# Kernel tuning notes

Measured on AMD Instinct MI355X. Metric: run time of the kernel, lower is better.

The kernel has to match this reference:

```python
import jax, jax.numpy as jnp
import numpy as np
from jax import lax

N, T, V, E, H, D, B = 16384, 16, 10000, 256, 256, 512, 128


def setup_inputs() -> dict:
    key = jax.random.key(0)
    ks = jax.random.split(key, 12)
    tok = jax.random.randint(ks[0], (N, T), 1, V)
    lens = jax.random.randint(ks[1], (N,), 4, T + 1)
    tok = jnp.where(jnp.arange(T)[None, :] < lens[:, None], tok, 0)  # pad_id = 0
    ast_path_len = jnp.full((B,), N // B, dtype=jnp.int32)  # 128 paths per sample
    u = lambda k, s: jax.random.uniform(k, s, jnp.float32, -0.1, 0.1)
    emb = u(ks[2], (V, E)).at[0].set(0.0)  # padding_idx=0 row zeroed
    return {
        "ast_path": tok,
        "ast_path_len": ast_path_len,
        "emb": emb,
        "W_ih_f": u(ks[3], (4 * H, E)), "W_hh_f": u(ks[4], (4 * H, H)), "b_f": u(ks[5], (4 * H,)),
        "W_ih_b": u(ks[6], (4 * H, E)), "W_hh_b": u(ks[7], (4 * H, H)), "b_b": u(ks[8], (4 * H,)),
        "W_lin": u(ks[9], (D, 2 * H)), "b_lin": jnp.zeros((D,), jnp.float32),
    }


def _lstm_final_h(x_tm, lens, W_ih, W_hh, b, reverse):
    # x_tm: [T, N, E]; returns final hidden state [N, H] honoring per-seq length
    n = x_tm.shape[1]
    h0 = jnp.zeros((n, H), x_tm.dtype)

    def step(carry, xt):
        h, c = carry
        x, t = xt
        gates = x @ W_ih.T + h @ W_hh.T + b  # [N, 4H]
        i, f, g, o = jnp.split(gates, 4, axis=-1)
        c_new = jax.nn.sigmoid(f) * c + jax.nn.sigmoid(i) * jnp.tanh(g)
        h_new = jax.nn.sigmoid(o) * jnp.tanh(c_new)
        m = (t < lens)[:, None]  # packed-sequence semantics: frozen past length
        return (jnp.where(m, h_new, h), jnp.where(m, c_new, c)), None

    (h, _), _ = lax.scan(step, (h0, h0), (x_tm, jnp.arange(x_tm.shape[0])), reverse=reverse)
    return h


def reference(ast_path, ast_path_len, emb, W_ih_f, W_hh_f, b_f, W_ih_b, W_hh_b, b_b, W_lin, b_lin):
    lens = (ast_path != 0).sum(axis=-1)  # pad_id = 0
    x = emb[ast_path]                     # [N, T, E]; dropout is identity at eval
    x_tm = jnp.swapaxes(x, 0, 1)          # [T, N, E]
    h_fwd = _lstm_final_h(x_tm, lens, W_ih_f, W_hh_f, b_f, reverse=False)
    h_bwd = _lstm_final_h(x_tm, lens, W_ih_b, W_hh_b, b_b, reverse=True)
    h_n = jnp.concatenate([h_fwd, h_bwd], axis=1)        # [N, 2H]
    repr_ = h_n @ W_lin.T + b_lin                         # [N, D]
    # segment-mean pooling over path groups (replaces the Python loop)
    n_paths = repr_.shape[0]
    seg_ids = jnp.repeat(jnp.arange(ast_path_len.shape[0]), ast_path_len,
                         total_repeat_length=n_paths)
    sums = jax.ops.segment_sum(repr_, seg_ids, num_segments=ast_path_len.shape[0])
    pooled = sums / ast_path_len[:, None].astype(repr_.dtype)  # [B, D]
    norm = jnp.sqrt(jnp.sum(pooled * pooled, axis=-1, keepdims=True))
    return pooled / jnp.maximum(norm, 1e-5)
```

## Files before the change

kernel.cpp:

```cpp
#include <hip/hip_runtime.h>
#include <stdint.h>

#define N_SEQ 16384
#define T_LEN 16
#define E_DIM 256
#define H_DIM 256
#define K_DIM 512
#define B_SAMP 128
#define V_SIZE 10000

typedef __bf16 bf16x8 __attribute__((ext_vector_type(8)));
typedef float  f32x4  __attribute__((ext_vector_type(4)));

__device__ __forceinline__ unsigned short f2bf(float x) {
  unsigned int u = __float_as_uint(x);
  u = (u + 0x7fffu + ((u >> 16) & 1u)) >> 16;
  return (unsigned short)u;
}
__device__ __forceinline__ float bf2f(unsigned short v) {
  return __uint_as_float(((unsigned int)v) << 16);
}
__device__ __forceinline__ float sigmoidf_(float x) {
  return 1.0f / (1.0f + __expf(-x));
}
__device__ __forceinline__ void glds16(const void* g, const void* l) {
  __builtin_amdgcn_global_load_lds(
      (const __attribute__((address_space(1))) unsigned int*)g,
      (__attribute__((address_space(3))) unsigned int*)l, 16, 0, 0);
}


__global__ __launch_bounds__(256) void k_lens(const int* __restrict__ tok, int* __restrict__ lens) {
  int n = blockIdx.x * 256 + threadIdx.x;
  const int* r = tok + n * T_LEN;
  int c = 0;
#pragma unroll
  for (int t = 0; t < T_LEN; ++t) c += (r[t] != 0);
  lens[n] = c;
}

__global__ __launch_bounds__(256) void k_hist(const int* __restrict__ lens, int* __restrict__ hist) {
  __shared__ int lh[17];
  if (threadIdx.x < 17) lh[threadIdx.x] = 0;
  __syncthreads();
  atomicAdd(&lh[lens[blockIdx.x * 256 + threadIdx.x]], 1);
  __syncthreads();
  if (threadIdx.x < 17) atomicAdd(&hist[threadIdx.x], lh[threadIdx.x]);
}

__global__ void k_offsets(const int* __restrict__ hist, int* __restrict__ cursor, int* __restrict__ cnts) {
  if (threadIdx.x == 0) {
    int off = 0;
    for (int l = 16; l >= 0; --l) { cursor[l] = off; off += hist[l]; }
    for (int t = 0; t < 16; ++t) {
      int c = 0;
      for (int l = t; l <= 16; ++l) c += hist[l];
      cnts[t] = c;
    }
  }
}

__global__ __launch_bounds__(256) void k_scatter(const int* __restrict__ lens, int* __restrict__ cursor,
                                                 int* __restrict__ perm, int* __restrict__ pinv,
                                                 int* __restrict__ plens) {
  int n = blockIdx.x * 256 + threadIdx.x;
  int l = lens[n];
  int pos = atomicAdd(&cursor[l], 1);
  perm[pos] = n;
  pinv[n] = pos;
  plens[pos] = l;
}

__global__ __launch_bounds__(256) void k_embcvt(const float* __restrict__ emb, unsigned short* __restrict__ out) {
  int i = blockIdx.x * 256 + threadIdx.x;
  out[i] = f2bf(emb[i]);
}

__global__ __launch_bounds__(256) void k_wprep(const float* __restrict__ Wih_f, const float* __restrict__ Whh_f,
                                               const float* __restrict__ Wih_b, const float* __restrict__ Whh_b,
                                               unsigned short* __restrict__ wpt_f, unsigned short* __restrict__ wpt_b) {
  int id = blockIdx.x * 256 + threadIdx.x;
  int dir = id >> 19;
  int rem = id & ((1 << 19) - 1);
  int p = rem >> 9;
  int k = rem & 511;
  int nb = p >> 8, wc = (p >> 6) & 3, q = (p >> 4) & 3, jj = p & 15;
  int r = q * 256 + nb * 64 + wc * 16 + jj;
  const float* Wih = dir ? Wih_b : Wih_f;
  const float* Whh = dir ? Whh_b : Whh_f;
  float v = (k < 256) ? Wih[r * 256 + k] : Whh[r * 256 + (k - 256)];
  unsigned short* o = dir ? wpt_b : wpt_f;
  o[p * 512 + k] = f2bf(v);
}


__global__ __launch_bounds__(512, 4)
void k_step(const unsigned short* __restrict__ embbf, const int* __restrict__ tok,
            const int* __restrict__ perm, const int* __restrict__ plens,
            const int* __restrict__ cnts,
            const unsigned short* __restrict__ wpt_f, const unsigned short* __restrict__ wpt_b,
            const float* __restrict__ bias_f, const float* __restrict__ bias_b,
            const unsigned short* __restrict__ hr_f, unsigned short* __restrict__ hw_f,
            const unsigned short* __restrict__ hr_b, unsigned short* __restrict__ hw_b,
            float* __restrict__ c_f, float* __restrict__ c_b,
            int s) {
  const int dir = blockIdx.y;
  const int t = dir ? (T_LEN - 1 - s) : s;
  const int mblk = blockIdx.x >> 2;
  const int m0 = mblk * 128;
  const int cnt = cnts[dir ? (15 - s) : s];
  if (m0 >= cnt) return;

  const int nblk = blockIdx.x & 3;
  const unsigned short* wpt = dir ? wpt_b : wpt_f;
  const float* bias = dir ? bias_b : bias_f;
  const unsigned short* hr = dir ? hr_b : hr_f;
  unsigned short* hw = dir ? hw_b : hw_f;
  float* cc = dir ? c_b : c_f;

  __shared__ __align__(128) unsigned char ldsA[128 * 128];
  __shared__ __align__(128) unsigned char ldsB[256 * 128];

  const int tid = threadIdx.x;
  const int lane = tid & 63;
  const int w = tid >> 6;
  const int wr = w >> 2;
  const int wc = w & 3;

  const int l8 = lane >> 3;
  const int l7 = lane & 7;
  const int arow0 = 16 * w + l8;
  const int arow1 = arow0 + 8;
  const int ach0 = l7 ^ (arow0 & 7);
  const int ach1 = l7 ^ (arow1 & 7);
  const int pn0 = perm[m0 + arow0];
  const int pn1 = perm[m0 + arow1];
  const unsigned aoffE0 = (unsigned)tok[pn0 * T_LEN + t] * E_DIM + ach0 * 8;
  const unsigned aoffE1 = (unsigned)tok[pn1 * T_LEN + t] * E_DIM + ach1 * 8;
  const unsigned aoffH0 = (unsigned)(m0 + arow0) * H_DIM + ach0 * 8;
  const unsigned aoffH1 = (unsigned)(m0 + arow1) * H_DIM + ach1 * 8;
  unsigned boff[4];
#pragma unroll
  for (int j = 0; j < 4; ++j) {
    const int brow = 32 * w + 8 * j + l8;
    const int bch = l7 ^ (brow & 7);
    boff[j] = (unsigned)(nblk * 256 + brow) * K_DIM + bch * 8;
  }

  f32x4 acc[4][4] = {};
  const int frow = lane & 15;
  const int fkq = lane >> 4;

  for (int kt = 0; kt < 8; ++kt) {
    const int k0 = kt * 64;
    if (kt < 4) {
      glds16(embbf + aoffE0 + k0, &ldsA[(16 * w) * 128]);
      glds16(embbf + aoffE1 + k0, &ldsA[(16 * w + 8) * 128]);
    } else {
      glds16(hr + aoffH0 + (k0 - E_DIM), &ldsA[(16 * w) * 128]);
      glds16(hr + aoffH1 + (k0 - E_DIM), &ldsA[(16 * w + 8) * 128]);
    }
#pragma unroll
    for (int j = 0; j < 4; ++j)
      glds16(wpt + boff[j] + k0, &ldsB[(32 * w + 8 * j) * 128]);
    __syncthreads();
#pragma unroll
    for (int ksub = 0; ksub < 2; ++ksub) {
      bf16x8 av[4], bv[4];
#pragma unroll
      for (int fr = 0; fr < 4; ++fr) {
        const int row = wr * 64 + fr * 16 + frow;
        const int ch = (ksub * 4 + fkq) ^ (row & 7);
        av[fr] = *(const bf16x8*)&ldsA[row * 128 + ch * 16];
      }
#pragma unroll
      for (int fc = 0; fc < 4; ++fc) {
        const int row = wc * 64 + fc * 16 + frow;
        const int ch = (ksub * 4 + fkq) ^ (row & 7);
        bv[fc] = *(const bf16x8*)&ldsB[row * 128 + ch * 16];
      }
#pragma unroll
      for (int fr = 0; fr < 4; ++fr)
#pragma unroll
        for (int fc = 0; fc < 4; ++fc)
          acc[fr][fc] = __builtin_amdgcn_mfma_f32_16x16x32_bf16(av[fr], bv[fc], acc[fr][fc], 0, 0, 0);
    }
    __syncthreads();
  }

  const int j = nblk * 64 + wc * 16 + frow;
  const float bi = bias[j], bfv = bias[256 + j], bg = bias[512 + j], bo = bias[768 + j];
#pragma unroll
  for (int fr = 0; fr < 4; ++fr) {
    const int nbase = m0 + wr * 64 + fr * 16 + fkq * 4;
    const int4 ln4 = *(const int4*)&plens[nbase];
    const f32x4 gi = acc[fr][0], gf = acc[fr][1], gg = acc[fr][2], go = acc[fr][3];
#pragma unroll
    for (int r = 0; r < 4; ++r) {
      const int n = nbase + r;
      const int ln = (r == 0) ? ln4.x : (r == 1) ? ln4.y : (r == 2) ? ln4.z : ln4.w;
      const size_t idx = (size_t)n * H_DIM + j;
      if (t < ln) {
        float iv = sigmoidf_(gi[r] + bi);
        float fv = sigmoidf_(gf[r] + bfv);
        float gv = tanhf(gg[r] + bg);
        float ov = sigmoidf_(go[r] + bo);
        float cn = fv * cc[idx] + iv * gv;
        cc[idx] = cn;
        hw[idx] = f2bf(ov * tanhf(cn));
      } else {
        hw[idx] = hr[idx];
      }
    }
  }
}


__global__ __launch_bounds__(256) void k_pool(const unsigned short* __restrict__ hf,
                                              const unsigned short* __restrict__ hb,
                                              const int* __restrict__ pinv,
                                              const int* __restrict__ plen,
                                              float* __restrict__ pooled) {
  const int b = blockIdx.x, tid = threadIdx.x;
  int start = 0;
  for (int i = 0; i < b; ++i) start += plen[i];
  const int cnt = plen[b];
  float s0 = 0.f, s1 = 0.f;
  for (int r = 0; r < cnt; ++r) {
    const size_t pr = (size_t)pinv[start + r];
    s0 += bf2f(hf[pr * H_DIM + tid]);
    s1 += bf2f(hb[pr * H_DIM + tid]);
  }
  float inv = 1.0f / (float)cnt;
  pooled[b * 512 + tid] = s0 * inv;
  pooled[b * 512 + H_DIM + tid] = s1 * inv;
}


__global__ __launch_bounds__(256) void k_final(const float* __restrict__ pooled,
                                               const float* __restrict__ W,
                                               const float* __restrict__ bl,
                                               float* __restrict__ out) {
  const int b = blockIdx.x, tid = threadIdx.x;
  __shared__ float pv[512];
  __shared__ float pre[512];
  __shared__ float red[4];
  pv[tid] = pooled[b * 512 + tid];
  pv[tid + 256] = pooled[b * 512 + 256 + tid];
  __syncthreads();
#pragma unroll
  for (int half = 0; half < 2; ++half) {
    const int dd = tid + half * 256;
    const f32x4* wr = (const f32x4*)(W + (size_t)dd * 512);
    const f32x4* pvv = (const f32x4*)pv;
    float s = bl[dd];
#pragma unroll 4
    for (int k4 = 0; k4 < 128; ++k4) {
      f32x4 wv = wr[k4], xv = pvv[k4];
      s += wv[0] * xv[0] + wv[1] * xv[1] + wv[2] * xv[2] + wv[3] * xv[3];
    }
    pre[dd] = s;
  }
  __syncthreads();
  float ss = pre[tid] * pre[tid] + pre[tid + 256] * pre[tid + 256];
#pragma unroll
  for (int off = 32; off > 0; off >>= 1) ss += __shfl_down(ss, off, 64);
  if ((tid & 63) == 0) red[tid >> 6] = ss;
  __syncthreads();
  float tot = red[0] + red[1] + red[2] + red[3];
  float scale = 1.0f / fmaxf(sqrtf(tot), 1e-5f);
  out[b * 512 + tid] = pre[tid] * scale;
  out[b * 512 + 256 + tid] = pre[tid + 256] * scale;
}


extern "C" void kernel_launch(void* const* d_in, const int* in_sizes, int n_in,
                              void* d_out, int out_size, void* d_ws, size_t ws_size,
                              hipStream_t stream) {
  const int* tok    = (const int*)d_in[0];
  const int* plen   = (const int*)d_in[1];
  const float* emb  = (const float*)d_in[2];
  const float* Wih_f = (const float*)d_in[3];
  const float* Whh_f = (const float*)d_in[4];
  const float* b_f   = (const float*)d_in[5];
  const float* Wih_b = (const float*)d_in[6];
  const float* Whh_b = (const float*)d_in[7];
  const float* b_b   = (const float*)d_in[8];
  const float* Wlin  = (const float*)d_in[9];
  const float* blin  = (const float*)d_in[10];
  float* out = (float*)d_out;

  char* ws = (char*)d_ws;
  size_t off = 0;
  auto alloc = [&](size_t bytes) {
    void* p = ws + off;
    off = (off + bytes + 255) & ~(size_t)255;
    return p;
  };
  unsigned short* embbf = (unsigned short*)alloc((size_t)V_SIZE * E_DIM * 2);
  unsigned short* wptf  = (unsigned short*)alloc((size_t)1024 * K_DIM * 2);
  unsigned short* wptb  = (unsigned short*)alloc((size_t)1024 * K_DIM * 2);
  int* lens             = (int*)alloc((size_t)N_SEQ * 4);
  int* perm             = (int*)alloc((size_t)N_SEQ * 4);
  int* pinv             = (int*)alloc((size_t)N_SEQ * 4);
  int* plens            = (int*)alloc((size_t)N_SEQ * 4);
  int* hist             = (int*)alloc(17 * 4);
  int* cursor           = (int*)alloc(17 * 4);
  int* cnts             = (int*)alloc(16 * 4);
  unsigned short* h0f   = (unsigned short*)alloc((size_t)N_SEQ * H_DIM * 2);
  unsigned short* h1f   = (unsigned short*)alloc((size_t)N_SEQ * H_DIM * 2);
  unsigned short* h0b   = (unsigned short*)alloc((size_t)N_SEQ * H_DIM * 2);
  unsigned short* h1b   = (unsigned short*)alloc((size_t)N_SEQ * H_DIM * 2);
  float* cf             = (float*)alloc((size_t)N_SEQ * H_DIM * 4);
  float* cb             = (float*)alloc((size_t)N_SEQ * H_DIM * 4);
  float* pooled         = (float*)alloc((size_t)B_SAMP * 512 * 4);

  hipMemsetAsync(hist, 0, 17 * 4, stream);
  hipMemsetAsync(h0f, 0, (size_t)N_SEQ * H_DIM * 2, stream);
  hipMemsetAsync(h0b, 0, (size_t)N_SEQ * H_DIM * 2, stream);
  hipMemsetAsync(h1f, 0, (size_t)N_SEQ * H_DIM * 2, stream);
  hipMemsetAsync(h1b, 0, (size_t)N_SEQ * H_DIM * 2, stream);
  hipMemsetAsync(cf, 0, (size_t)N_SEQ * H_DIM * 4, stream);
  hipMemsetAsync(cb, 0, (size_t)N_SEQ * H_DIM * 4, stream);

  k_lens<<<N_SEQ / 256, 256, 0, stream>>>(tok, lens);
  k_hist<<<N_SEQ / 256, 256, 0, stream>>>(lens, hist);
  k_offsets<<<1, 64, 0, stream>>>(hist, cursor, cnts);
  k_scatter<<<N_SEQ / 256, 256, 0, stream>>>(lens, cursor, perm, pinv, plens);
  k_embcvt<<<(V_SIZE * E_DIM) / 256, 256, 0, stream>>>(emb, embbf);
  k_wprep<<<(2 * 1024 * K_DIM) / 256, 256, 0, stream>>>(Wih_f, Whh_f, Wih_b, Whh_b, wptf, wptb);

  dim3 grid(512, 2);
  for (int s = 0; s < T_LEN; ++s) {
    const unsigned short* hrf = (s & 1) ? h1f : h0f;
    unsigned short* hwf       = (s & 1) ? h0f : h1f;
    const unsigned short* hrb = (s & 1) ? h1b : h0b;
    unsigned short* hwb       = (s & 1) ? h0b : h1b;
    k_step<<<grid, 512, 0, stream>>>(embbf, tok, perm, plens, cnts, wptf, wptb, b_f, b_b,
                                     hrf, hwf, hrb, hwb, cf, cb, s);
  }
  k_pool<<<B_SAMP, 256, 0, stream>>>(h0f, h0b, pinv, plen, pooled);
  k_final<<<B_SAMP, 256, 0, stream>>>(pooled, Wlin, blin, out);
}
```

Measured before the change: 943.6 us.

## Fuse per-timestep LSTM launches into one persistent kernel with on-chip state

Replaces the 16 per-timestep k_step launches with a single k_lstm kernel. Each block owns 64 length-sorted rows for one direction and loops over that block's maximum length. The hidden state stays in swizzled LDS and the cell state stays in registers, which removes the global h/c ping-pong buffers, their memsets, and the per-step launch overhead. Weights are now streamed from global/L2 by every block on every step, so cache traffic is higher. Blocks are paired across directions to balance the sorted lengths, and tanh is replaced with an exp-based approximation.

```diff
diff --git a/kernel.cpp b/kernel.cpp
--- a/kernel.cpp
+++ b/kernel.cpp
@@ -11,17 +11,23 @@
 
 typedef __bf16 bf16x8 __attribute__((ext_vector_type(8)));
 typedef float  f32x4  __attribute__((ext_vector_type(4)));
-
-__device__ __forceinline__ unsigned short f2bf(float x) {
+typedef unsigned short u16x8 __attribute__((ext_vector_type(8)));
+typedef unsigned short ush;
+
+__device__ __forceinline__ ush f2bf(float x) {
   unsigned int u = __float_as_uint(x);
   u = (u + 0x7fffu + ((u >> 16) & 1u)) >> 16;
-  return (unsigned short)u;
-}
-__device__ __forceinline__ float bf2f(unsigned short v) {
+  return (ush)u;
+}
+__device__ __forceinline__ float bf2f(ush v) {
   return __uint_as_float(((unsigned int)v) << 16);
 }
 __device__ __forceinline__ float sigmoidf_(float x) {
   return 1.0f / (1.0f + __expf(-x));
+}
+__device__ __forceinline__ float tanhf_(float x) {
+  float e = __expf(2.0f * x);
+  return 1.0f - 2.0f / (e + 1.0f);
 }
 __device__ __forceinline__ void glds16(const void* g, const void* l) {
   __builtin_amdgcn_global_load_lds(
@@ -48,15 +54,10 @@
   if (threadIdx.x < 17) atomicAdd(&hist[threadIdx.x], lh[threadIdx.x]);
 }
 
-__global__ void k_offsets(const int* __restrict__ hist, int* __restrict__ cursor, int* __restrict__ cnts) {
+__global__ void k_offsets(const int* __restrict__ hist, int* __restrict__ cursor) {
   if (threadIdx.x == 0) {
     int off = 0;
     for (int l = 16; l >= 0; --l) { cursor[l] = off; off += hist[l]; }
-    for (int t = 0; t < 16; ++t) {
-      int c = 0;
-      for (int l = t; l <= 16; ++l) c += hist[l];
-      cnts[t] = c;
-    }
   }
 }
 
@@ -71,153 +72,174 @@
   plens[pos] = l;
 }
 
-__global__ __launch_bounds__(256) void k_embcvt(const float* __restrict__ emb, unsigned short* __restrict__ out) {
+__global__ __launch_bounds__(256) void k_embcvt(const float* __restrict__ emb, ush* __restrict__ out) {
   int i = blockIdx.x * 256 + threadIdx.x;
   out[i] = f2bf(emb[i]);
 }
 
 __global__ __launch_bounds__(256) void k_wprep(const float* __restrict__ Wih_f, const float* __restrict__ Whh_f,
                                                const float* __restrict__ Wih_b, const float* __restrict__ Whh_b,
-                                               unsigned short* __restrict__ wpt_f, unsigned short* __restrict__ wpt_b) {
+                                               ush* __restrict__ wpt_f, ush* __restrict__ wpt_b) {
   int id = blockIdx.x * 256 + threadIdx.x;
   int dir = id >> 19;
   int rem = id & ((1 << 19) - 1);
   int p = rem >> 9;
   int k = rem & 511;
-  int nb = p >> 8, wc = (p >> 6) & 3, q = (p >> 4) & 3, jj = p & 15;
-  int r = q * 256 + nb * 64 + wc * 16 + jj;
+  int nc = p >> 8, w = (p >> 6) & 3, q = (p >> 4) & 3, jj = p & 15;
+  int r = q * 256 + nc * 64 + w * 16 + jj;
   const float* Wih = dir ? Wih_b : Wih_f;
   const float* Whh = dir ? Whh_b : Whh_f;
   float v = (k < 256) ? Wih[r * 256 + k] : Whh[r * 256 + (k - 256)];
-  unsigned short* o = dir ? wpt_b : wpt_f;
+  ush* o = dir ? wpt_b : wpt_f;
   o[p * 512 + k] = f2bf(v);
 }
 
 
-__global__ __launch_bounds__(512, 4)
-void k_step(const unsigned short* __restrict__ embbf, const int* __restrict__ tok,
+__global__ __launch_bounds__(256, 2)
+void k_lstm(const ush* __restrict__ embbf, const int* __restrict__ tok,
             const int* __restrict__ perm, const int* __restrict__ plens,
-            const int* __restrict__ cnts,
-            const unsigned short* __restrict__ wpt_f, const unsigned short* __restrict__ wpt_b,
+            const ush* __restrict__ wpt_f, const ush* __restrict__ wpt_b,
             const float* __restrict__ bias_f, const float* __restrict__ bias_b,
-            const unsigned short* __restrict__ hr_f, unsigned short* __restrict__ hw_f,
-            const unsigned short* __restrict__ hr_b, unsigned short* __restrict__ hw_b,
-            float* __restrict__ c_f, float* __restrict__ c_b,
-            int s) {
-  const int dir = blockIdx.y;
-  const int t = dir ? (T_LEN - 1 - s) : s;
-  const int mblk = blockIdx.x >> 2;
-  const int m0 = mblk * 128;
-  const int cnt = cnts[dir ? (15 - s) : s];
-  if (m0 >= cnt) return;
-
-  const int nblk = blockIdx.x & 3;
-  const unsigned short* wpt = dir ? wpt_b : wpt_f;
+            ush* __restrict__ hfin_f, ush* __restrict__ hfin_b) {
+  const int bi = blockIdx.x;
+  int rb, dir;
+  if (bi < 256) { rb = bi; dir = bi & 1; }
+  else          { rb = 511 - bi; dir = 1 - (rb & 1); }
+  const int m0 = rb * 64;
+  const ush* wpt = dir ? wpt_b : wpt_f;
   const float* bias = dir ? bias_b : bias_f;
-  const unsigned short* hr = dir ? hr_b : hr_f;
-  unsigned short* hw = dir ? hw_b : hw_f;
-  float* cc = dir ? c_b : c_f;
-
-  __shared__ __align__(128) unsigned char ldsA[128 * 128];
-  __shared__ __align__(128) unsigned char ldsB[256 * 128];
+  ush* hfin = dir ? hfin_b : hfin_f;
+
+  __shared__ __align__(128) ush xs[64 * 256];
+  __shared__ __align__(128) ush hs[64 * 256];
 
   const int tid = threadIdx.x;
   const int lane = tid & 63;
   const int w = tid >> 6;
-  const int wr = w >> 2;
-  const int wc = w & 3;
-
-  const int l8 = lane >> 3;
-  const int l7 = lane & 7;
-  const int arow0 = 16 * w + l8;
-  const int arow1 = arow0 + 8;
-  const int ach0 = l7 ^ (arow0 & 7);
-  const int ach1 = l7 ^ (arow1 & 7);
-  const int pn0 = perm[m0 + arow0];
-  const int pn1 = perm[m0 + arow1];
-  const unsigned aoffE0 = (unsigned)tok[pn0 * T_LEN + t] * E_DIM + ach0 * 8;
-  const unsigned aoffE1 = (unsigned)tok[pn1 * T_LEN + t] * E_DIM + ach1 * 8;
-  const unsigned aoffH0 = (unsigned)(m0 + arow0) * H_DIM + ach0 * 8;
-  const unsigned aoffH1 = (unsigned)(m0 + arow1) * H_DIM + ach1 * 8;
-  unsigned boff[4];
-#pragma unroll
-  for (int j = 0; j < 4; ++j) {
-    const int brow = 32 * w + 8 * j + l8;
-    const int bch = l7 ^ (brow & 7);
-    boff[j] = (unsigned)(nblk * 256 + brow) * K_DIM + bch * 8;
-  }
-
-  f32x4 acc[4][4] = {};
-  const int frow = lane & 15;
-  const int fkq = lane >> 4;
-
-  for (int kt = 0; kt < 8; ++kt) {
-    const int k0 = kt * 64;
-    if (kt < 4) {
-      glds16(embbf + aoffE0 + k0, &ldsA[(16 * w) * 128]);
-      glds16(embbf + aoffE1 + k0, &ldsA[(16 * w + 8) * 128]);
-    } else {
-      glds16(hr + aoffH0 + (k0 - E_DIM), &ldsA[(16 * w) * 128]);
-      glds16(hr + aoffH1 + (k0 - E_DIM), &ldsA[(16 * w + 8) * 128]);
+  const int frow = lane & 15, fkq = lane >> 4;
+  const int maxlen = plens[m0];
+
+  int4 ln[4];
+#pragma unroll
+  for (int fr = 0; fr < 4; ++fr) ln[fr] = *(const int4*)&plens[m0 + fr * 16 + fkq * 4];
+
+  {
+    u16x8 z = {};
+#pragma unroll
+    for (int i = 0; i < 8; ++i) *(u16x8*)&hs[(i * 256 + tid) * 8] = z;
+  }
+  f32x4 c4[4][4] = {};
+  uint2 hn[4][4];
+
+  const int xrow_base = w * 16 + (lane >> 5);
+  const int xch = lane & 31;
+  const int jl = w * 16 + frow;
+
+  auto flushh = [&](int tp) {
+#pragma unroll
+    for (int nc = 0; nc < 4; ++nc) {
+      const int j = nc * 64 + jl;
+      const int hch = j >> 3, jb = j & 7;
+#pragma unroll
+      for (int fr = 0; fr < 4; ++fr) {
+        const int nl = fr * 16 + fkq * 4;
+        const uint2 pk = hn[nc][fr];
+        if (tp < ln[fr].x) hs[(nl + 0) * 256 + ((hch ^ ((nl + 0) & 7)) * 8) + jb] = (ush)(pk.x & 0xffffu);
+        if (tp < ln[fr].y) hs[(nl + 1) * 256 + ((hch ^ ((nl + 1) & 7)) * 8) + jb] = (ush)(pk.x >> 16);
+        if (tp < ln[fr].z) hs[(nl + 2) * 256 + ((hch ^ ((nl + 2) & 7)) * 8) + jb] = (ush)(pk.y & 0xffffu);
+        if (tp < ln[fr].w) hs[(nl + 3) * 256 + ((hch ^ ((nl + 3) & 7)) * 8) + jb] = (ush)(pk.y >> 16);
+      }
     }
-#pragma unroll
-    for (int j = 0; j < 4; ++j)
-      glds16(wpt + boff[j] + k0, &ldsB[(32 * w + 8 * j) * 128]);
+  };
+
+  for (int s = 0; s < maxlen; ++s) {
+    const int t = dir ? (maxlen - 1 - s) : s;
     __syncthreads();
-#pragma unroll
-    for (int ksub = 0; ksub < 2; ++ksub) {
-      bf16x8 av[4], bv[4];
-#pragma unroll
-      for (int fr = 0; fr < 4; ++fr) {
-        const int row = wr * 64 + fr * 16 + frow;
-        const int ch = (ksub * 4 + fkq) ^ (row & 7);
-        av[fr] = *(const bf16x8*)&ldsA[row * 128 + ch * 16];
-      }
-#pragma unroll
-      for (int fc = 0; fc < 4; ++fc) {
-        const int row = wc * 64 + fc * 16 + frow;
-        const int ch = (ksub * 4 + fkq) ^ (row & 7);
-        bv[fc] = *(const bf16x8*)&ldsB[row * 128 + ch * 16];
-      }
-#pragma unroll
-      for (int fr = 0; fr < 4; ++fr)
-#pragma unroll
-        for (int fc = 0; fc < 4; ++fc)
-          acc[fr][fc] = __builtin_amdgcn_mfma_f32_16x16x32_bf16(av[fr], bv[fc], acc[fr][fc], 0, 0, 0);
+    if (s > 0) flushh(dir ? (maxlen - s) : (s - 1));
+#pragma unroll
+    for (int q = 0; q < 8; ++q) {
+      const int row = xrow_base + q * 2;
+      const int pn = perm[m0 + row];
+      const int tokv = tok[pn * T_LEN + t];
+      glds16(embbf + (size_t)tokv * 256 + ((xch ^ (row & 7)) * 8), xs + (w * 8 + q) * 512);
     }
     __syncthreads();
-  }
-
-  const int j = nblk * 64 + wc * 16 + frow;
-  const float bi = bias[j], bfv = bias[256 + j], bg = bias[512 + j], bo = bias[768 + j];
-#pragma unroll
-  for (int fr = 0; fr < 4; ++fr) {
-    const int nbase = m0 + wr * 64 + fr * 16 + fkq * 4;
-    const int4 ln4 = *(const int4*)&plens[nbase];
-    const f32x4 gi = acc[fr][0], gf = acc[fr][1], gg = acc[fr][2], go = acc[fr][3];
-#pragma unroll
-    for (int r = 0; r < 4; ++r) {
-      const int n = nbase + r;
-      const int ln = (r == 0) ? ln4.x : (r == 1) ? ln4.y : (r == 2) ? ln4.z : ln4.w;
-      const size_t idx = (size_t)n * H_DIM + j;
-      if (t < ln) {
-        float iv = sigmoidf_(gi[r] + bi);
-        float fv = sigmoidf_(gf[r] + bfv);
-        float gv = tanhf(gg[r] + bg);
-        float ov = sigmoidf_(go[r] + bo);
-        float cn = fv * cc[idx] + iv * gv;
-        cc[idx] = cn;
-        hw[idx] = f2bf(ov * tanhf(cn));
-      } else {
-        hw[idx] = hr[idx];
+
+#pragma unroll
+    for (int nc = 0; nc < 4; ++nc) {
+      const int j = nc * 64 + jl;
+      f32x4 acc[4][4];
+#pragma unroll
+      for (int q = 0; q < 4; ++q) {
+        const float bq = bias[q * 256 + j];
+#pragma unroll
+        for (int fr = 0; fr < 4; ++fr) acc[fr][q] = f32x4{bq, bq, bq, bq};
+      }
+#pragma unroll 2
+      for (int kc = 0; kc < 16; ++kc) {
+        bf16x8 bv[4];
+#pragma unroll
+        for (int q = 0; q < 4; ++q) {
+          const int prow = nc * 256 + w * 64 + q * 16 + frow;
+          bv[q] = *(const bf16x8*)&wpt[(size_t)prow * 512 + kc * 32 + fkq * 8];
+        }
+        bf16x8 av[4];
+        const ush* abase = (kc < 8) ? xs : hs;
+        const int kcl = kc & 7;
+#pragma unroll
+        for (int fr = 0; fr < 4; ++fr) {
+          const int row = fr * 16 + frow;
+          const int cch = (kcl * 4 + fkq) ^ (row & 7);
+          av[fr] = *(const bf16x8*)&abase[row * 256 + cch * 8];
+        }
+#pragma unroll
+        for (int fr = 0; fr < 4; ++fr)
+#pragma unroll
+          for (int q = 0; q < 4; ++q)
+            acc[fr][q] = __builtin_amdgcn_mfma_f32_16x16x32_bf16(av[fr], bv[q], acc[fr][q], 0, 0, 0);
+      }
+#pragma unroll
+      for (int fr = 0; fr < 4; ++fr) {
+        unsigned int pk0 = 0, pk1 = 0;
+#pragma unroll
+        for (int r = 0; r < 4; ++r) {
+          const int lnv = (r == 0) ? ln[fr].x : (r == 1) ? ln[fr].y : (r == 2) ? ln[fr].z : ln[fr].w;
+          float hv = 0.0f;
+          if (t < lnv) {
+            const float iv = sigmoidf_(acc[fr][0][r]);
+            const float fv = sigmoidf_(acc[fr][1][r]);
+            const float gv = tanhf_(acc[fr][2][r]);
+            const float ov = sigmoidf_(acc[fr][3][r]);
+            const float cn = fv * c4[nc][fr][r] + iv * gv;
+            c4[nc][fr][r] = cn;
+            hv = ov * tanhf_(cn);
+          }
+          const unsigned int hb = f2bf(hv);
+          if (r == 0) pk0 |= hb;
+          else if (r == 1) pk0 |= hb << 16;
+          else if (r == 2) pk1 |= hb;
+          else pk1 |= hb << 16;
+        }
+        hn[nc][fr] = make_uint2(pk0, pk1);
       }
     }
   }
-}
-
-
-__global__ __launch_bounds__(256) void k_pool(const unsigned short* __restrict__ hf,
-                                              const unsigned short* __restrict__ hb,
+
+  __syncthreads();
+  flushh(dir ? 0 : (maxlen - 1));
+  __syncthreads();
+#pragma unroll
+  for (int i = 0; i < 8; ++i) {
+    const int g = i * 256 + tid;
+    const int row = g >> 5, ch = g & 31;
+    u16x8 v = *(const u16x8*)&hs[row * 256 + ((ch ^ (row & 7)) * 8)];
+    *(u16x8*)&hfin[(size_t)(m0 + row) * 256 + ch * 8] = v;
+  }
+}
+
+
+__global__ __launch_bounds__(256) void k_pool(const ush* __restrict__ hf,
+                                              const ush* __restrict__ hb,
                                               const int* __restrict__ pinv,
                                               const int* __restrict__ plen,
                                               float* __restrict__ pooled) {
@@ -297,48 +319,30 @@
     off = (off + bytes + 255) & ~(size_t)255;
     return p;
   };
-  unsigned short* embbf = (unsigned short*)alloc((size_t)V_SIZE * E_DIM * 2);
-  unsigned short* wptf  = (unsigned short*)alloc((size_t)1024 * K_DIM * 2);
-  unsigned short* wptb  = (unsigned short*)alloc((size_t)1024 * K_DIM * 2);
-  int* lens             = (int*)alloc((size_t)N_SEQ * 4);
-  int* perm             = (int*)alloc((size_t)N_SEQ * 4);
-  int* pinv             = (int*)alloc((size_t)N_SEQ * 4);
-  int* plens            = (int*)alloc((size_t)N_SEQ * 4);
-  int* hist             = (int*)alloc(17 * 4);
-  int* cursor           = (int*)alloc(17 * 4);
-  int* cnts             = (int*)alloc(16 * 4);
-  unsigned short* h0f   = (unsigned short*)alloc((size_t)N_SEQ * H_DIM * 2);
-  unsigned short* h1f   = (unsigned short*)alloc((size_t)N_SEQ * H_DIM * 2);
-  unsigned short* h0b   = (unsigned short*)alloc((size_t)N_SEQ * H_DIM * 2);
-  unsigned short* h1b   = (unsigned short*)alloc((size_t)N_SEQ * H_DIM * 2);
-  float* cf             = (float*)alloc((size_t)N_SEQ * H_DIM * 4);
-  float* cb             = (float*)alloc((size_t)N_SEQ * H_DIM * 4);
-  float* pooled         = (float*)alloc((size_t)B_SAMP * 512 * 4);
+  ush* embbf = (ush*)alloc((size_t)V_SIZE * E_DIM * 2);
+  ush* wptf  = (ush*)alloc((size_t)1024 * K_DIM * 2);
+  ush* wptb  = (ush*)alloc((size_t)1024 * K_DIM * 2);
+  int* lens  = (int*)alloc((size_t)N_SEQ * 4);
+  int* perm  = (int*)alloc((size_t)N_SEQ * 4);
+  int* pinv  = (int*)alloc((size_t)N_SEQ * 4);
+  int* plens = (int*)alloc((size_t)N_SEQ * 4);
+  int* hist  = (int*)alloc(17 * 4);
+  int* cursor = (int*)alloc(17 * 4);
+  ush* hfinf = (ush*)alloc((size_t)N_SEQ * H_DIM * 2);
+  ush* hfinb = (ush*)alloc((size_t)N_SEQ * H_DIM * 2);
+  float* pooled = (float*)alloc((size_t)B_SAMP * 512 * 4);
 
   hipMemsetAsync(hist, 0, 17 * 4, stream);
-  hipMemsetAsync(h0f, 0, (size_t)N_SEQ * H_DIM * 2, stream);
-  hipMemsetAsync(h0b, 0, (size_t)N_SEQ * H_DIM * 2, stream);
-  hipMemsetAsync(h1f, 0, (size_t)N_SEQ * H_DIM * 2, stream);
-  hipMemsetAsync(h1b, 0, (size_t)N_SEQ * H_DIM * 2, stream);
-  hipMemsetAsync(cf, 0, (size_t)N_SEQ * H_DIM * 4, stream);
-  hipMemsetAsync(cb, 0, (size_t)N_SEQ * H_DIM * 4, stream);
 
   k_lens<<<N_SEQ / 256, 256, 0, stream>>>(tok, lens);
   k_hist<<<N_SEQ / 256, 256, 0, stream>>>(lens, hist);
-  k_offsets<<<1, 64, 0, stream>>>(hist, cursor, cnts);
+  k_offsets<<<1, 64, 0, stream>>>(hist, cursor);
   k_scatter<<<N_SEQ / 256, 256, 0, stream>>>(lens, cursor, perm, pinv, plens);
   k_embcvt<<<(V_SIZE * E_DIM) / 256, 256, 0, stream>>>(emb, embbf);
   k_wprep<<<(2 * 1024 * K_DIM) / 256, 256, 0, stream>>>(Wih_f, Whh_f, Wih_b, Whh_b, wptf, wptb);
 
-  dim3 grid(512, 2);
-  for (int s = 0; s < T_LEN; ++s) {
-    const unsigned short* hrf = (s & 1) ? h1f : h0f;
-    unsigned short* hwf       = (s & 1) ? h0f : h1f;
-    const unsigned short* hrb = (s & 1) ? h1b : h0b;
-    unsigned short* hwb       = (s & 1) ? h0b : h1b;
-    k_step<<<grid, 512, 0, stream>>>(embbf, tok, perm, plens, cnts, wptf, wptb, b_f, b_b,
-                                     hrf, hwf, hrb, hwb, cf, cb, s);
-  }
-  k_pool<<<B_SAMP, 256, 0, stream>>>(h0f, h0b, pinv, plen, pooled);
+  k_lstm<<<512, 256, 0, stream>>>(embbf, tok, perm, plens, wptf, wptb, b_f, b_b, hfinf, hfinb);
+
+  k_pool<<<B_SAMP, 256, 0, stream>>>(hfinf, hfinb, pinv, plen, pooled);
   k_final<<<B_SAMP, 256, 0, stream>>>(pooled, Wlin, blin, out);
 }
```

Result: slower. 1.160 ms (+22.9%).

## Transpose cell state, precompute permuted tokens, skip frozen backward rows, fuse histogram

Applied to the files above, without the earlier changes.

The cell state is stored transposed (hidden × sequence), so each thread reads and writes four cell values with one vector access. The cell state is reset inline on each sequence's first valid step, which removes its memsets. A precomputed time-major permuted token table replaces the per-step perm→tok double gather. Backward-direction blocks skip sequences that are frozen and no longer copy their hidden state; forward keeps the copy because of ping-pong buffering. Also: the lens and histogram kernels are fused, tanh uses a fast exp-based formula with some accuracy risk, MFMA issue priority is raised via setprio, and the grid interleaves both directions in a 1D launch.

```diff
diff --git a/kernel.cpp b/kernel.cpp
--- a/kernel.cpp
+++ b/kernel.cpp
@@ -11,17 +11,22 @@
 
 typedef __bf16 bf16x8 __attribute__((ext_vector_type(8)));
 typedef float  f32x4  __attribute__((ext_vector_type(4)));
-
-__device__ __forceinline__ unsigned short f2bf(float x) {
+typedef unsigned short ush;
+
+__device__ __forceinline__ ush f2bf(float x) {
   unsigned int u = __float_as_uint(x);
   u = (u + 0x7fffu + ((u >> 16) & 1u)) >> 16;
-  return (unsigned short)u;
-}
-__device__ __forceinline__ float bf2f(unsigned short v) {
+  return (ush)u;
+}
+__device__ __forceinline__ float bf2f(ush v) {
   return __uint_as_float(((unsigned int)v) << 16);
 }
 __device__ __forceinline__ float sigmoidf_(float x) {
   return 1.0f / (1.0f + __expf(-x));
+}
+__device__ __forceinline__ float tanhf_(float x) {
+  float e = __expf(2.0f * x);
+  return 1.0f - 2.0f / (e + 1.0f);
 }
 __device__ __forceinline__ void glds16(const void* g, const void* l) {
   __builtin_amdgcn_global_load_lds(
@@ -30,32 +35,33 @@
 }
 
 
-__global__ __launch_bounds__(256) void k_lens(const int* __restrict__ tok, int* __restrict__ lens) {
+__global__ __launch_bounds__(256) void k_lens(const int* __restrict__ tok, int* __restrict__ lens,
+                                              int* __restrict__ hist) {
+  __shared__ int lh[17];
+  if (threadIdx.x < 17) lh[threadIdx.x] = 0;
+  __syncthreads();
   int n = blockIdx.x * 256 + threadIdx.x;
   const int* r = tok + n * T_LEN;
   int c = 0;
 #pragma unroll
   for (int t = 0; t < T_LEN; ++t) c += (r[t] != 0);
   lens[n] = c;
-}
-
-__global__ __launch_bounds__(256) void k_hist(const int* __restrict__ lens, int* __restrict__ hist) {
-  __shared__ int lh[17];
-  if (threadIdx.x < 17) lh[threadIdx.x] = 0;
-  __syncthreads();
-  atomicAdd(&lh[lens[blockIdx.x * 256 + threadIdx.x]], 1);
-  __syncthreads();
-  if (threadIdx.x < 17) atomicAdd(&hist[threadIdx.x], lh[threadIdx.x]);
-}
-
-__global__ void k_offsets(const int* __restrict__ hist, int* __restrict__ cursor, int* __restrict__ cnts) {
+  atomicAdd(&lh[c], 1);
+  __syncthreads();
+  if (threadIdx.x < 17 && lh[threadIdx.x]) atomicAdd(&hist[threadIdx.x], lh[threadIdx.x]);
+}
+
+__global__ void k_offsets(const int* __restrict__ hist, int* __restrict__ cursor,
+                          int* __restrict__ cnts_f, int* __restrict__ cnts_b) {
   if (threadIdx.x == 0) {
     int off = 0;
     for (int l = 16; l >= 0; --l) { cursor[l] = off; off += hist[l]; }
     for (int t = 0; t < 16; ++t) {
-      int c = 0;
-      for (int l = t; l <= 16; ++l) c += hist[l];
-      cnts[t] = c;
+      int cf = 0, cb = 0;
+      for (int l = t; l <= 16; ++l) cf += hist[l];
+      for (int l = t + 1; l <= 16; ++l) cb += hist[l];
+      cnts_f[t] = cf;
+      cnts_b[t] = cb;
     }
   }
 }
@@ -71,14 +77,22 @@
   plens[pos] = l;
 }
 
-__global__ __launch_bounds__(256) void k_embcvt(const float* __restrict__ emb, unsigned short* __restrict__ out) {
+__global__ __launch_bounds__(256) void k_tokperm(const int* __restrict__ tok, const int* __restrict__ perm,
+                                                 int* __restrict__ tokperm) {
+  int id = blockIdx.x * 256 + threadIdx.x;
+  int t = id >> 14;
+  int pos = id & (N_SEQ - 1);
+  tokperm[id] = tok[perm[pos] * T_LEN + t];
+}
+
+__global__ __launch_bounds__(256) void k_embcvt(const float* __restrict__ emb, ush* __restrict__ out) {
   int i = blockIdx.x * 256 + threadIdx.x;
   out[i] = f2bf(emb[i]);
 }
 
 __global__ __launch_bounds__(256) void k_wprep(const float* __restrict__ Wih_f, const float* __restrict__ Whh_f,
                                                const float* __restrict__ Wih_b, const float* __restrict__ Whh_b,
-                                               unsigned short* __restrict__ wpt_f, unsigned short* __restrict__ wpt_b) {
+                                               ush* __restrict__ wpt_f, ush* __restrict__ wpt_b) {
   int id = blockIdx.x * 256 + threadIdx.x;
   int dir = id >> 19;
   int rem = id & ((1 << 19) - 1);
@@ -89,34 +103,35 @@
   const float* Wih = dir ? Wih_b : Wih_f;
   const float* Whh = dir ? Whh_b : Whh_f;
   float v = (k < 256) ? Wih[r * 256 + k] : Whh[r * 256 + (k - 256)];
-  unsigned short* o = dir ? wpt_b : wpt_f;
+  ush* o = dir ? wpt_b : wpt_f;
   o[p * 512 + k] = f2bf(v);
 }
 
 
 __global__ __launch_bounds__(512, 4)
-void k_step(const unsigned short* __restrict__ embbf, const int* __restrict__ tok,
-            const int* __restrict__ perm, const int* __restrict__ plens,
-            const int* __restrict__ cnts,
-            const unsigned short* __restrict__ wpt_f, const unsigned short* __restrict__ wpt_b,
+void k_step(const ush* __restrict__ embbf, const int* __restrict__ tokperm,
+            const int* __restrict__ plens,
+            const int* __restrict__ cnts_f, const int* __restrict__ cnts_b,
+            const ush* __restrict__ wpt_f, const ush* __restrict__ wpt_b,
             const float* __restrict__ bias_f, const float* __restrict__ bias_b,
-            const unsigned short* __restrict__ hr_f, unsigned short* __restrict__ hw_f,
-            const unsigned short* __restrict__ hr_b, unsigned short* __restrict__ hw_b,
-            float* __restrict__ c_f, float* __restrict__ c_b,
+            const ush* __restrict__ hr_f, ush* __restrict__ hw_f,
+            const ush* __restrict__ hr_b, ush* __restrict__ hw_b,
+            float* __restrict__ cT_f, float* __restrict__ cT_b,
             int s) {
-  const int dir = blockIdx.y;
-  const int t = dir ? (T_LEN - 1 - s) : s;
-  const int mblk = blockIdx.x >> 2;
-  const int m0 = mblk * 128;
-  const int cnt = cnts[dir ? (15 - s) : s];
+  const int b = blockIdx.x;
+  const int dir = b & 1;
+  const int nblk = (b & 7) >> 1;
+  const int rt = b >> 3;
+  const int t = dir ? (15 - s) : s;
+  const int cnt = dir ? cnts_b[t] : cnts_f[t];
+  const int m0 = rt * 128;
   if (m0 >= cnt) return;
 
-  const int nblk = blockIdx.x & 3;
-  const unsigned short* wpt = dir ? wpt_b : wpt_f;
+  const ush* wpt = dir ? wpt_b : wpt_f;
   const float* bias = dir ? bias_b : bias_f;
-  const unsigned short* hr = dir ? hr_b : hr_f;
-  unsigned short* hw = dir ? hw_b : hw_f;
-  float* cc = dir ? c_b : c_f;
+  const ush* hr = dir ? hr_b : hr_f;
+  ush* hw = dir ? hw_b : hw_f;
+  float* cT = dir ? cT_b : cT_f;
 
   __shared__ __align__(128) unsigned char ldsA[128 * 128];
   __shared__ __align__(128) unsigned char ldsB[256 * 128];
@@ -133,10 +148,8 @@
   const int arow1 = arow0 + 8;
   const int ach0 = l7 ^ (arow0 & 7);
   const int ach1 = l7 ^ (arow1 & 7);
-  const int pn0 = perm[m0 + arow0];
-  const int pn1 = perm[m0 + arow1];
-  const unsigned aoffE0 = (unsigned)tok[pn0 * T_LEN + t] * E_DIM + ach0 * 8;
-  const unsigned aoffE1 = (unsigned)tok[pn1 * T_LEN + t] * E_DIM + ach1 * 8;
+  const unsigned aoffE0 = (unsigned)tokperm[t * N_SEQ + m0 + arow0] * E_DIM + ach0 * 8;
+  const unsigned aoffE1 = (unsigned)tokperm[t * N_SEQ + m0 + arow1] * E_DIM + ach1 * 8;
   const unsigned aoffH0 = (unsigned)(m0 + arow0) * H_DIM + ach0 * 8;
   const unsigned aoffH1 = (unsigned)(m0 + arow1) * H_DIM + ach1 * 8;
   unsigned boff[4];
@@ -179,45 +192,49 @@
         const int ch = (ksub * 4 + fkq) ^ (row & 7);
         bv[fc] = *(const bf16x8*)&ldsB[row * 128 + ch * 16];
       }
+      __builtin_amdgcn_s_setprio(1);
 #pragma unroll
       for (int fr = 0; fr < 4; ++fr)
 #pragma unroll
         for (int fc = 0; fc < 4; ++fc)
           acc[fr][fc] = __builtin_amdgcn_mfma_f32_16x16x32_bf16(av[fr], bv[fc], acc[fr][fc], 0, 0, 0);
+      __builtin_amdgcn_s_setprio(0);
     }
     __syncthreads();
   }
 
   const int j = nblk * 64 + wc * 16 + frow;
-  const float bi = bias[j], bfv = bias[256 + j], bg = bias[512 + j], bo = bias[768 + j];
+  const float b0 = bias[j], b1 = bias[256 + j], b2 = bias[512 + j], b3 = bias[768 + j];
 #pragma unroll
   for (int fr = 0; fr < 4; ++fr) {
-    const int nbase = m0 + wr * 64 + fr * 16 + fkq * 4;
-    const int4 ln4 = *(const int4*)&plens[nbase];
+    const int n0 = m0 + wr * 64 + fr * 16 + fkq * 4;
+    const int4 l4 = *(const int4*)&plens[n0];
+    f32x4 cv = *(const f32x4*)&cT[(size_t)j * N_SEQ + n0];
     const f32x4 gi = acc[fr][0], gf = acc[fr][1], gg = acc[fr][2], go = acc[fr][3];
 #pragma unroll
     for (int r = 0; r < 4; ++r) {
-      const int n = nbase + r;
-      const int ln = (r == 0) ? ln4.x : (r == 1) ? ln4.y : (r == 2) ? ln4.z : ln4.w;
-      const size_t idx = (size_t)n * H_DIM + j;
-      if (t < ln) {
-        float iv = sigmoidf_(gi[r] + bi);
-        float fv = sigmoidf_(gf[r] + bfv);
-        float gv = tanhf(gg[r] + bg);
-        float ov = sigmoidf_(go[r] + bo);
-        float cn = fv * cc[idx] + iv * gv;
-        cc[idx] = cn;
-        hw[idx] = f2bf(ov * tanhf(cn));
-      } else {
-        hw[idx] = hr[idx];
+      const int lnv = (r == 0) ? l4.x : (r == 1) ? l4.y : (r == 2) ? l4.z : l4.w;
+      const size_t hidx = (size_t)(n0 + r) * H_DIM + j;
+      if (t < lnv) {
+        const float iv = sigmoidf_(gi[r] + b0);
+        const float fv = sigmoidf_(gf[r] + b1);
+        const float gv = tanhf_(gg[r] + b2);
+        const float ov = sigmoidf_(go[r] + b3);
+        const bool first = dir ? (t == lnv - 1) : (t == 0);
+        const float cn = fv * (first ? 0.0f : cv[r]) + iv * gv;
+        cv[r] = cn;
+        hw[hidx] = f2bf(ov * tanhf_(cn));
+      } else if (!dir) {
+        hw[hidx] = hr[hidx];
       }
     }
-  }
-}
-
-
-__global__ __launch_bounds__(256) void k_pool(const unsigned short* __restrict__ hf,
-                                              const unsigned short* __restrict__ hb,
+    *(f32x4*)&cT[(size_t)j * N_SEQ + n0] = cv;
+  }
+}
+
+
+__global__ __launch_bounds__(256) void k_pool(const ush* __restrict__ hf,
+                                              const ush* __restrict__ hb,
                                               const int* __restrict__ pinv,
                                               const int* __restrict__ plen,
                                               float* __restrict__ pooled) {
@@ -297,47 +314,46 @@
     off = (off + bytes + 255) & ~(size_t)255;
     return p;
   };
-  unsigned short* embbf = (unsigned short*)alloc((size_t)V_SIZE * E_DIM * 2);
-  unsigned short* wptf  = (unsigned short*)alloc((size_t)1024 * K_DIM * 2);
-  unsigned short* wptb  = (unsigned short*)alloc((size_t)1024 * K_DIM * 2);
-  int* lens             = (int*)alloc((size_t)N_SEQ * 4);
-  int* perm             = (int*)alloc((size_t)N_SEQ * 4);
-  int* pinv             = (int*)alloc((size_t)N_SEQ * 4);
-  int* plens            = (int*)alloc((size_t)N_SEQ * 4);
-  int* hist             = (int*)alloc(17 * 4);
-  int* cursor           = (int*)alloc(17 * 4);
-  int* cnts             = (int*)alloc(16 * 4);
-  unsigned short* h0f   = (unsigned short*)alloc((size_t)N_SEQ * H_DIM * 2);
-  unsigned short* h1f   = (unsigned short*)alloc((size_t)N_SEQ * H_DIM * 2);
-  unsigned short* h0b   = (unsigned short*)alloc((size_t)N_SEQ * H_DIM * 2);
-  unsigned short* h1b   = (unsigned short*)alloc((size_t)N_SEQ * H_DIM * 2);
-  float* cf             = (float*)alloc((size_t)N_SEQ * H_DIM * 4);
-  float* cb             = (float*)alloc((size_t)N_SEQ * H_DIM * 4);
-  float* pooled         = (float*)alloc((size_t)B_SAMP * 512 * 4);
+  ush* embbf   = (ush*)alloc((size_t)V_SIZE * E_DIM * 2);
+  ush* wptf    = (ush*)alloc((size_t)1024 * K_DIM * 2);
+  ush* wptb    = (ush*)alloc((size_t)1024 * K_DIM * 2);
+  int* lens    = (int*)alloc((size_t)N_SEQ * 4);
+  int* perm    = (int*)alloc((size_t)N_SEQ * 4);
+  int* pinv    = (int*)alloc((size_t)N_SEQ * 4);
+  int* plens   = (int*)alloc((size_t)N_SEQ * 4);
+  int* tokperm = (int*)alloc((size_t)T_LEN * N_SEQ * 4);
+  int* hist    = (int*)alloc(17 * 4);
+  int* cursor  = (int*)alloc(17 * 4);
+  int* cntsf   = (int*)alloc(16 * 4);
+  int* cntsb   = (int*)alloc(16 * 4);
+  ush* h0f     = (ush*)alloc((size_t)N_SEQ * H_DIM * 2);
+  ush* h1f     = (ush*)alloc((size_t)N_SEQ * H_DIM * 2);
+  ush* h0b     = (ush*)alloc((size_t)N_SEQ * H_DIM * 2);
+  ush* h1b     = (ush*)alloc((size_t)N_SEQ * H_DIM * 2);
+  float* cTf   = (float*)alloc((size_t)H_DIM * N_SEQ * 4);
+  float* cTb   = (float*)alloc((size_t)H_DIM * N_SEQ * 4);
+  float* pooled = (float*)alloc((size_t)B_SAMP * 512 * 4);
 
   hipMemsetAsync(hist, 0, 17 * 4, stream);
   hipMemsetAsync(h0f, 0, (size_t)N_SEQ * H_DIM * 2, stream);
+  hipMemsetAsync(h1f, 0, (size_t)N_SEQ * H_DIM * 2, stream);
   hipMemsetAsync(h0b, 0, (size_t)N_SEQ * H_DIM * 2, stream);
-  hipMemsetAsync(h1f, 0, (size_t)N_SEQ * H_DIM * 2, stream);
   hipMemsetAsync(h1b, 0, (size_t)N_SEQ * H_DIM * 2, stream);
-  hipMemsetAsync(cf, 0, (size_t)N_SEQ * H_DIM * 4, stream);
-  hipMemsetAsync(cb, 0, (size_t)N_SEQ * H_DIM * 4, stream);
-
-  k_lens<<<N_SEQ / 256, 256, 0, stream>>>(tok, lens);
-  k_hist<<<N_SEQ / 256, 256, 0, stream>>>(lens, hist);
-  k_offsets<<<1, 64, 0, stream>>>(hist, cursor, cnts);
+
+  k_lens<<<N_SEQ / 256, 256, 0, stream>>>(tok, lens, hist);
+  k_offsets<<<1, 64, 0, stream>>>(hist, cursor, cntsf, cntsb);
   k_scatter<<<N_SEQ / 256, 256, 0, stream>>>(lens, cursor, perm, pinv, plens);
+  k_tokperm<<<(T_LEN * N_SEQ) / 256, 256, 0, stream>>>(tok, perm, tokperm);
   k_embcvt<<<(V_SIZE * E_DIM) / 256, 256, 0, stream>>>(emb, embbf);
   k_wprep<<<(2 * 1024 * K_DIM) / 256, 256, 0, stream>>>(Wih_f, Whh_f, Wih_b, Whh_b, wptf, wptb);
 
-  dim3 grid(512, 2);
   for (int s = 0; s < T_LEN; ++s) {
-    const unsigned short* hrf = (s & 1) ? h1f : h0f;
-    unsigned short* hwf       = (s & 1) ? h0f : h1f;
-    const unsigned short* hrb = (s & 1) ? h1b : h0b;
-    unsigned short* hwb       = (s & 1) ? h0b : h1b;
-    k_step<<<grid, 512, 0, stream>>>(embbf, tok, perm, plens, cnts, wptf, wptb, b_f, b_b,
-                                     hrf, hwf, hrb, hwb, cf, cb, s);
+    const ush* hrf = (s & 1) ? h1f : h0f;
+    ush* hwf       = (s & 1) ? h0f : h1f;
+    const ush* hrb = (s & 1) ? h1b : h0b;
+    ush* hwb       = (s & 1) ? h0b : h1b;
+    k_step<<<1024, 512, 0, stream>>>(embbf, tokperm, plens, cntsf, cntsb, wptf, wptb,
+                                     b_f, b_b, hrf, hwf, hrb, hwb, cTf, cTb, s);
   }
   k_pool<<<B_SAMP, 256, 0, stream>>>(h0f, h0b, pinv, plen, pooled);
   k_final<<<B_SAMP, 256, 0, stream>>>(pooled, Wlin, blin, out);
```

Result: no change. 936.2 us (-0.8%).
